# Kernel tuning notes

Hardware: AMD Instinct MI355X
Metric: run time of the kernel (lower is better)

Reference implementation:

```python
import jax, jax.numpy as jnp
import numpy as np

# SMPL-style 24-joint kinematic tree (parents[j] < j, root has parent -1)
PARENTS = [-1, 0, 0, 0, 1, 2, 3, 4, 5, 6, 7, 8, 9, 9, 9, 12, 13, 14, 16, 17, 18, 19, 20, 21]
B, J = 524288, 24


def setup_inputs() -> dict:
    key = jax.random.key(0)
    k1, k2 = jax.random.split(key)
    rotations = jax.random.normal(k1, (B, J, 4), dtype=jnp.float32)
    initial_skeleton = jax.random.normal(k2, (J, 3), dtype=jnp.float32)
    return {"rotations": rotations, "initial_skeleton": initial_skeleton}


def quat_to_matrix(q):
    # q: [..., 4] (w, x, y, z) -> R: [..., 3, 3]. Faithful to the torch code
    # (no normalization of the quaternion).
    w, x, y, z = q[..., 0], q[..., 1], q[..., 2], q[..., 3]
    r00 = 1 - 2 * (y * y + z * z)
    r01 = 2 * (x * y - z * w)
    r02 = 2 * (x * z + y * w)
    r10 = 2 * (x * y + z * w)
    r11 = 1 - 2 * (x * x + z * z)
    r12 = 2 * (y * z - x * w)
    r20 = 2 * (x * z - y * w)
    r21 = 2 * (y * z + x * w)
    r22 = 1 - 2 * (x * x + y * y)
    row0 = jnp.stack([r00, r01, r02], axis=-1)
    row1 = jnp.stack([r10, r11, r12], axis=-1)
    row2 = jnp.stack([r20, r21, r22], axis=-1)
    return jnp.stack([row0, row1, row2], axis=-2)


def reference(rotations, initial_skeleton):
    # rotations: [B, J, 4] -> joints: [B, J, 3]
    parents = np.asarray(PARENTS)
    # Per-joint bone offset in rest pose; root gets skel[0]-skel[0] = 0.
    offsets = initial_skeleton - initial_skeleton[np.maximum(parents, 0)]  # [J, 3]
    R = quat_to_matrix(rotations)                                          # [B, J, 3, 3]
    # Rotate each bone offset by the joint's own rotation (as in the source),
    # fully parallel across batch and joints.
    rotated = jnp.einsum('bjik,jk->bji', R, offsets)                       # [B, J, 3]
    # Accumulate along the tree (J=24 is a small structural loop).
    b = rotations.shape[0]
    pos = [None] * len(parents)
    pos[0] = jnp.zeros((b, 3), dtype=rotations.dtype)
    for j in range(1, len(parents)):
        pos[j] = pos[parents[j]] + rotated[:, j]
    return jnp.stack(pos, axis=1)  # [B, J, 3]
```

## Files before the change

kernel.cpp:

```cpp
#include <hip/hip_runtime.h>

typedef float floatx4 __attribute__((ext_vector_type(4)));

__device__ __constant__ int cA1[24] = {0,0,0,0,1,2,3,4,5,6,7,8,9,9,9,12,13,14,16,17,18,19,20,21};
__device__ __constant__ int cA2[24] = {0,0,0,0,0,0,0,1,2,3,4,5,6,6,6,9,9,9,13,14,16,17,18,19};
__device__ __constant__ int cA3[24] = {0,0,0,0,0,0,0,0,0,0,1,2,3,3,3,6,6,6,9,9,13,14,16,17};
__device__ __constant__ int cA4[24] = {0,0,0,0,0,0,0,0,0,0,0,0,0,0,0,3,3,3,6,6,9,9,13,14};

#define ITERS 16

__device__ __forceinline__ void qrot_acc(const float4 q,
                                         const float ox, const float oy, const float oz,
                                         float& vx, float& vy, float& vz) {
    const float w = q.x, x = q.y, y = q.z, z = q.w;
    vx += (1.f - 2.f * (y * y + z * z)) * ox + (2.f * (x * y - z * w)) * oy + (2.f * (x * z + y * w)) * oz;
    vy += (2.f * (x * y + z * w)) * ox + (1.f - 2.f * (x * x + z * z)) * oy + (2.f * (y * z - x * w)) * oz;
    vz += (2.f * (x * z - y * w)) * ox + (2.f * (y * z + x * w)) * oy + (1.f - 2.f * (x * x + y * y)) * oz;
}

__global__ __launch_bounds__(256, 4) void fk_kernel(
    const float* __restrict__ rot,
    const float* __restrict__ skel,
    float* __restrict__ out,
    int B)
{
    const int tid = threadIdx.x;
    const int j   = tid & 31;
    const int grp = tid >> 5;
    const int jc  = (j < 24) ? j : 0;

    const int a1 = cA1[jc], a2 = cA2[jc], a3 = cA3[jc], a4 = cA4[jc];

    const float sJx = skel[jc * 3 + 0], sJy = skel[jc * 3 + 1], sJz = skel[jc * 3 + 2];
    const float s1x = skel[a1 * 3 + 0], s1y = skel[a1 * 3 + 1], s1z = skel[a1 * 3 + 2];
    const float s2x = skel[a2 * 3 + 0], s2y = skel[a2 * 3 + 1], s2z = skel[a2 * 3 + 2];
    const float s3x = skel[a3 * 3 + 0], s3y = skel[a3 * 3 + 1], s3z = skel[a3 * 3 + 2];
    const float s4x = skel[a4 * 3 + 0], s4y = skel[a4 * 3 + 1], s4z = skel[a4 * 3 + 2];
    const float oSx = sJx - s1x, oSy = sJy - s1y, oSz = sJz - s1z;
    const float o1x = s1x - s2x, o1y = s1y - s2y, o1z = s1z - s2z;
    const float o2x = s2x - s3x, o2y = s2y - s3y, o2z = s2z - s3z;
    const float o3x = s3x - s4x, o3y = s3y - s4y, o3z = s3z - s4z;

    const int sA = (4 * j) / 3;
    const int sB = (sA < 23) ? sA + 1 : 23;
    const int r  = j % 3;

    const float4* __restrict__ rot4 = reinterpret_cast<const float4*>(rot);
    floatx4* __restrict__ out4 = reinterpret_cast<floatx4*>(out);

    const int base = blockIdx.x * (8 * ITERS);

#pragma unroll 4
    for (int it = 0; it < ITERS; ++it) {
        const int b = base + it * 8 + grp;
        if (b < B) {
            const size_t b24 = (size_t)b * 24;
            const float4 qS = rot4[b24 + jc];
            const float4 q1 = rot4[b24 + a1];
            const float4 q2 = rot4[b24 + a2];
            const float4 q3 = rot4[b24 + a3];

            float vx = 0.f, vy = 0.f, vz = 0.f;
            qrot_acc(qS, oSx, oSy, oSz, vx, vy, vz);
            qrot_acc(q1, o1x, o1y, o1z, vx, vy, vz);
            qrot_acc(q2, o2x, o2y, o2z, vx, vy, vz);
            qrot_acc(q3, o3x, o3y, o3z, vx, vy, vz);

            const float cx = vx + __shfl(vx, a4, 32);
            const float cy = vy + __shfl(vy, a4, 32);
            const float cz = vz + __shfl(vz, a4, 32);

            const float axA = __shfl(cx, sA, 32), ayA = __shfl(cy, sA, 32), azA = __shfl(cz, sA, 32);
            const float axB = __shfl(cx, sB, 32), ayB = __shfl(cy, sB, 32), azB = __shfl(cz, sB, 32);

            const float o0 = (r == 0) ? axA : (r == 1) ? ayA : azA;
            const float o1 = (r == 0) ? ayA : (r == 1) ? azA : axB;
            const float o2 = (r == 0) ? azA : (r == 1) ? axB : ayB;
            const float o3 = (r == 0) ? axB : (r == 1) ? ayB : azB;

            if (j < 18) {
                floatx4 v; v.x = o0; v.y = o1; v.z = o2; v.w = o3;
                __builtin_nontemporal_store(v, out4 + (size_t)b * 18 + j);
            }
        }
    }
}

extern "C" void kernel_launch(void* const* d_in, const int* in_sizes, int n_in,
                              void* d_out, int out_size, void* d_ws, size_t ws_size,
                              hipStream_t stream) {
    const float* rot  = (const float*)d_in[0];
    const float* skel = (const float*)d_in[1];
    float* out = (float*)d_out;

    const int B = in_sizes[0] / (24 * 4);
    const int perBlock = 8 * ITERS;
    const int grid = (B + perBlock - 1) / perBlock;
    fk_kernel<<<grid, 256, 0, stream>>>(rot, skel, out, B);
}
```

Measured before the change: 71.90 us.

## Cut per-joint quaternion loads and repack output with ds_permute

Each joint lane now loads only its own quaternion and its parent's, instead of four ancestors. The remaining ancestor contributions come from two pointer-jumping shuffle rounds, first via the grandparent and then via the great-great-grandparent. The six shuffles plus selects used to pack xyz into float4 output are replaced by four ds_permute pushes with precomputed addresses and component selectors. Launch bounds are raised to allow more waves per CU. This reduces redundant global and cache loads and rotation arithmetic, but adds a shuffle round to the dependent chain.

```diff
diff --git a/kernel.cpp b/kernel.cpp
--- a/kernel.cpp
+++ b/kernel.cpp
@@ -4,7 +4,6 @@
 
 __device__ __constant__ int cA1[24] = {0,0,0,0,1,2,3,4,5,6,7,8,9,9,9,12,13,14,16,17,18,19,20,21};
 __device__ __constant__ int cA2[24] = {0,0,0,0,0,0,0,1,2,3,4,5,6,6,6,9,9,9,13,14,16,17,18,19};
-__device__ __constant__ int cA3[24] = {0,0,0,0,0,0,0,0,0,0,1,2,3,3,3,6,6,6,9,9,13,14,16,17};
 __device__ __constant__ int cA4[24] = {0,0,0,0,0,0,0,0,0,0,0,0,0,0,0,3,3,3,6,6,9,9,13,14};
 
 #define ITERS 16
@@ -18,7 +17,18 @@
     vz += (2.f * (x * z - y * w)) * ox + (2.f * (y * z + x * w)) * oy + (1.f - 2.f * (x * x + y * y)) * oz;
 }
 
-__global__ __launch_bounds__(256, 4) void fk_kernel(
+__device__ __forceinline__ void repack_const(int r, int j, int wavehalf,
+                                             int& addr, int& comp) {
+    int c = (r - 3 * j) & 3;
+    int d;
+    if (j < 24 && c < 3) { d = (3 * j + c) >> 2; }
+    else if (j < 24)     { d = 18 + (j >> 2); c = 0; }
+    else                 { d = j; c = 0; }
+    addr = (wavehalf + d) << 2;
+    comp = c;
+}
+
+__global__ __launch_bounds__(256, 8) void fk_kernel(
     const float* __restrict__ rot,
     const float* __restrict__ skel,
     float* __restrict__ out,
@@ -28,22 +38,21 @@
     const int j   = tid & 31;
     const int grp = tid >> 5;
     const int jc  = (j < 24) ? j : 0;
+    const int wavehalf = tid & 32;
 
-    const int a1 = cA1[jc], a2 = cA2[jc], a3 = cA3[jc], a4 = cA4[jc];
+    const int a1 = cA1[jc], a2 = cA2[jc], a4 = cA4[jc];
 
     const float sJx = skel[jc * 3 + 0], sJy = skel[jc * 3 + 1], sJz = skel[jc * 3 + 2];
     const float s1x = skel[a1 * 3 + 0], s1y = skel[a1 * 3 + 1], s1z = skel[a1 * 3 + 2];
     const float s2x = skel[a2 * 3 + 0], s2y = skel[a2 * 3 + 1], s2z = skel[a2 * 3 + 2];
-    const float s3x = skel[a3 * 3 + 0], s3y = skel[a3 * 3 + 1], s3z = skel[a3 * 3 + 2];
-    const float s4x = skel[a4 * 3 + 0], s4y = skel[a4 * 3 + 1], s4z = skel[a4 * 3 + 2];
     const float oSx = sJx - s1x, oSy = sJy - s1y, oSz = sJz - s1z;
-    const float o1x = s1x - s2x, o1y = s1y - s2y, o1z = s1z - s2z;
-    const float o2x = s2x - s3x, o2y = s2y - s3y, o2z = s2z - s3z;
-    const float o3x = s3x - s4x, o3y = s3y - s4y, o3z = s3z - s4z;
+    const float oPx = s1x - s2x, oPy = s1y - s2y, oPz = s1z - s2z;
 
-    const int sA = (4 * j) / 3;
-    const int sB = (sA < 23) ? sA + 1 : 23;
-    const int r  = j % 3;
+    int ad0, cp0, ad1, cp1, ad2, cp2, ad3, cp3;
+    repack_const(0, j, wavehalf, ad0, cp0);
+    repack_const(1, j, wavehalf, ad1, cp1);
+    repack_const(2, j, wavehalf, ad2, cp2);
+    repack_const(3, j, wavehalf, ad3, cp3);
 
     const float4* __restrict__ rot4 = reinterpret_cast<const float4*>(rot);
     floatx4* __restrict__ out4 = reinterpret_cast<floatx4*>(out);
@@ -56,27 +65,29 @@
         if (b < B) {
             const size_t b24 = (size_t)b * 24;
             const float4 qS = rot4[b24 + jc];
-            const float4 q1 = rot4[b24 + a1];
-            const float4 q2 = rot4[b24 + a2];
-            const float4 q3 = rot4[b24 + a3];
+            const float4 qP = rot4[b24 + a1];
 
             float vx = 0.f, vy = 0.f, vz = 0.f;
             qrot_acc(qS, oSx, oSy, oSz, vx, vy, vz);
-            qrot_acc(q1, o1x, o1y, o1z, vx, vy, vz);
-            qrot_acc(q2, o2x, o2y, o2z, vx, vy, vz);
-            qrot_acc(q3, o3x, o3y, o3z, vx, vy, vz);
+            qrot_acc(qP, oPx, oPy, oPz, vx, vy, vz);
 
-            const float cx = vx + __shfl(vx, a4, 32);
-            const float cy = vy + __shfl(vy, a4, 32);
-            const float cz = vz + __shfl(vz, a4, 32);
+            const float x2 = vx + __shfl(vx, a2, 32);
+            const float y2 = vy + __shfl(vy, a2, 32);
+            const float z2 = vz + __shfl(vz, a2, 32);
 
-            const float axA = __shfl(cx, sA, 32), ayA = __shfl(cy, sA, 32), azA = __shfl(cz, sA, 32);
-            const float axB = __shfl(cx, sB, 32), ayB = __shfl(cy, sB, 32), azB = __shfl(cz, sB, 32);
+            const float cx = x2 + __shfl(x2, a4, 32);
+            const float cy = y2 + __shfl(y2, a4, 32);
+            const float cz = z2 + __shfl(z2, a4, 32);
 
-            const float o0 = (r == 0) ? axA : (r == 1) ? ayA : azA;
-            const float o1 = (r == 0) ? ayA : (r == 1) ? azA : axB;
-            const float o2 = (r == 0) ? azA : (r == 1) ? axB : ayB;
-            const float o3 = (r == 0) ? axB : (r == 1) ? ayB : azB;
+            const float s0 = (cp0 == 0) ? cx : (cp0 == 1) ? cy : cz;
+            const float s1 = (cp1 == 0) ? cx : (cp1 == 1) ? cy : cz;
+            const float s2 = (cp2 == 0) ? cx : (cp2 == 1) ? cy : cz;
+            const float s3 = (cp3 == 0) ? cx : (cp3 == 1) ? cy : cz;
+
+            const float o0 = __int_as_float(__builtin_amdgcn_ds_permute(ad0, __float_as_int(s0)));
+            const float o1 = __int_as_float(__builtin_amdgcn_ds_permute(ad1, __float_as_int(s1)));
+            const float o2 = __int_as_float(__builtin_amdgcn_ds_permute(ad2, __float_as_int(s2)));
+            const float o3 = __int_as_float(__builtin_amdgcn_ds_permute(ad3, __float_as_int(s3)));
 
             if (j < 18) {
                 floatx4 v; v.x = o0; v.y = o1; v.z = o2; v.w = o3;
```

New measurement: 58.93 us. 18.0% less time.
